# Kernel optimization log

Hardware: AMD Instinct MI355X
Metric: run time of the kernel (lower is better)

Reference implementation:

```python
import jax, jax.numpy as jnp
import numpy as np

N = 200000   # nodes
E = 500000   # edges
B = 4096     # batch of events
K = 20       # temporal neighbors
M = 100000   # pending raw messages
D = 128      # node feat / embedding dim
DT = 128     # time encoding dim (= D in TGN)
DM = 128     # memory dim
MSG = 128    # message dim
RAW = 2 * DM + D + DT   # 512 raw message dim
HID = RAW // 2          # 256 mlp hidden
HEADS = 2
QD = D + DT             # 256 attention query dim (= MHA embed_dim)
KD = D + DT + D         # 384 attention key dim (neigh feat + time + edge feat)
DH = QD // HEADS


def setup_inputs() -> dict:
    key = jax.random.key(0)
    ks = jax.random.split(key, 40)
    f = lambda i, shape, s=0.05: jax.random.normal(ks[i], shape, jnp.float32) * s
    ri = lambda i, shape, hi: jax.random.randint(ks[i], shape, 0, hi, jnp.int32)
    return {
        # event batch (int constants)
        'src_nodes': ri(0, (B,), N), 'dst_nodes': ri(1, (B,), N), 'neg_nodes': ri(2, (B,), N),
        'edge_times': ri(3, (B,), 1000000),
        # temporal neighbor lists for the 3B query nodes (neighbor_finder output)
        'neighbors': ri(4, (3 * B, K), N),
        'neighbor_edge_idxs': ri(5, (3 * B, K), E),
        'neighbor_edge_times': ri(6, (3 * B, K), 1000000),
        # pending raw message events ('last' aggregator picks last per node)
        'msg_src': ri(7, (M,), N), 'msg_dst': ri(8, (M,), N),
        'msg_eidx': ri(9, (M,), E), 'msg_t': ri(10, (M,), 1000000),
        'last_update': ri(11, (N,), 500000),
        # learned params / state (floats)
        'node_feats': f(12, (N, D)), 'edge_feats': f(13, (E, D)), 'memory': f(14, (N, DM)),
        'time_w': f(15, (DT,), 1.0), 'time_b': f(16, (DT,), 1.0),
        'msg_W1': f(17, (HID, RAW)), 'msg_b1': f(18, (HID,)),
        'msg_W2': f(19, (MSG, HID)), 'msg_b2': f(20, (MSG,)),
        'gru_Wi': f(21, (3 * DM, MSG)), 'gru_Wh': f(22, (3 * DM, DM)),
        'gru_bi': f(23, (3 * DM,)), 'gru_bh': f(24, (3 * DM,)),
        'Wq': f(25, (QD, QD)), 'bq': f(26, (QD,)),
        'Wk': f(27, (QD, KD)), 'bk': f(28, (QD,)),
        'Wv': f(29, (QD, KD)), 'bv': f(30, (QD,)),
        'Wo': f(31, (QD, QD)), 'bo': f(32, (QD,)),
        'mW1': f(33, (D, QD + D)), 'mb1': f(34, (D,)),
        'mW2': f(35, (D, D)), 'mb2': f(36, (D,)),
    }


def _time_enc(t, w, b):
    # TimeEncode: cos(t * w + b); t [...], out [..., DT]
    return jnp.cos(t[..., None] * w + b)


def _forward(node_feats, edge_feats, memory, time_w, time_b,
             msg_W1, msg_b1, msg_W2, msg_b2,
             gru_Wi, gru_Wh, gru_bi, gru_bh,
             Wq, bq, Wk, bk, Wv, bv, Wo, bo, mW1, mb1, mW2, mb2,
             src_nodes, dst_nodes, neg_nodes, edge_times,
             neighbors, neighbor_edge_idxs, neighbor_edge_times,
             msg_src, msg_dst, msg_eidx, msg_t, last_update):
    # ---- 1. get_updated_memory: 'last' aggregator + mlp message fn + GRU ----
    pos = jnp.arange(M, dtype=jnp.int32)
    last_pos = jnp.full((N,), -1, jnp.int32).at[msg_src].max(pos)  # last msg per node
    has_msg = last_pos >= 0
    idx = jnp.maximum(last_pos, 0)
    s, d = msg_src[idx], msg_dst[idx]
    e, t = msg_eidx[idx], msg_t[idx]
    dt = (t - last_update[s]).astype(jnp.float32)
    raw = jnp.concatenate([memory[s], memory[d], edge_feats[e],
                           _time_enc(dt, time_w, time_b)], axis=-1)  # [N, RAW]
    h1 = jax.nn.relu(raw @ msg_W1.T + msg_b1)
    msg = h1 @ msg_W2.T + msg_b2                                    # [N, MSG]
    # torch GRUCell (gate order r, z, n)
    gi = msg @ gru_Wi.T + gru_bi
    gh = memory @ gru_Wh.T + gru_bh
    ir, iz, inn = jnp.split(gi, 3, axis=-1)
    hr, hz, hn = jnp.split(gh, 3, axis=-1)
    r = jax.nn.sigmoid(ir + hr)
    z = jax.nn.sigmoid(iz + hz)
    n = jnp.tanh(inn + r * hn)
    new_mem = (1.0 - z) * n + z * memory
    mem_upd = jnp.where(has_msg[:, None], new_mem, memory)          # [N, DM]

    # ---- 2. graph-attention embedding (1 layer) over temporal neighbors ----
    nodes = jnp.concatenate([src_nodes, dst_nodes, neg_nodes])      # [3B]
    ts = jnp.tile(edge_times, 3).astype(jnp.float32)                # [3B]
    src_feat = mem_upd[nodes] + node_feats[nodes]                   # [3B, D]
    q_in = jnp.concatenate([src_feat,
                            _time_enc(jnp.zeros_like(ts), time_w, time_b)], -1)  # [3B, QD]
    pad_mask = neighbors == 0                                       # TGN: id 0 = padding
    n_feat = mem_upd[neighbors] + node_feats[neighbors]             # [3B, K, D]
    dt_n = ts[:, None] - neighbor_edge_times.astype(jnp.float32)
    k_in = jnp.concatenate([n_feat, _time_enc(dt_n, time_w, time_b),
                            edge_feats[neighbor_edge_idxs]], -1)    # [3B, K, KD]
    q = (q_in @ Wq.T + bq).reshape(-1, HEADS, DH)                   # [3B, H, DH]
    k = (k_in @ Wk.T + bk).reshape(-1, K, HEADS, DH)
    v = (k_in @ Wv.T + bv).reshape(-1, K, HEADS, DH)
    scores = jnp.einsum('bhd,bkhd->bhk', q, k) / jnp.sqrt(jnp.float32(DH))
    scores = jnp.where(pad_mask[:, None, :], -1e9, scores)
    attn = jax.nn.softmax(scores, axis=-1)                          # [3B, H, K]
    ctx = jnp.einsum('bhk,bkhd->bhd', attn, v).reshape(-1, QD)
    attn_out = ctx @ Wo.T + bo                                      # [3B, QD]
    all_masked = jnp.all(pad_mask, axis=-1)
    attn_out = jnp.where(all_masked[:, None], 0.0, attn_out)
    # MergeLayer(attn_out, src_feat)
    h = jax.nn.relu(jnp.concatenate([attn_out, src_feat], -1) @ mW1.T + mb1)
    emb = h @ mW2.T + mb2                                           # [3B, D]
    return emb.reshape(3, B, D)  # (source, destination, negative) embeddings


def reference(src_nodes, dst_nodes, neg_nodes, edge_times, neighbors,
              neighbor_edge_idxs, neighbor_edge_times, msg_src, msg_dst,
              msg_eidx, msg_t, last_update, node_feats, edge_feats, memory,
              time_w, time_b, msg_W1, msg_b1, msg_W2, msg_b2, gru_Wi, gru_Wh,
              gru_bi, gru_bh, Wq, bq, Wk, bk, Wv, bv, Wo, bo, mW1, mb1, mW2, mb2):
    return _forward(node_feats, edge_feats, memory, time_w, time_b,
                    msg_W1, msg_b1, msg_W2, msg_b2,
                    gru_Wi, gru_Wh, gru_bi, gru_bh,
                    Wq, bq, Wk, bk, Wv, bv, Wo, bo, mW1, mb1, mW2, mb2,
                    src_nodes, dst_nodes, neg_nodes, edge_times,
                    neighbors, neighbor_edge_idxs, neighbor_edge_times,
                    msg_src, msg_dst, msg_eidx, msg_t, last_update)
```

## Files before the change

kernel.cpp:

```cpp
#include <hip/hip_runtime.h>
#include <math.h>

#define NN 200000
#define EEDGE 500000
#define BB 4096
#define KK 20
#define MM 100000
#define Q3 (3*BB)
#define NBLK ((NN + 255) / 256)

typedef _Float16 __attribute__((ext_vector_type(8))) f16x8;
typedef _Float16 __attribute__((ext_vector_type(4))) f16x4;
typedef float __attribute__((ext_vector_type(4))) f32x4;

#define MFMA16(a,b,c) __builtin_amdgcn_mfma_f32_16x16x32_f16(a,b,c,0,0,0)

__device__ __forceinline__ float fast_cos(float a) {
    double ad = (double)a * 0.15915494309189535;
    double fr = ad - floor(ad);
    return __builtin_amdgcn_cosf((float)fr);
}

__device__ __forceinline__ float tenc(float dt, float w, float b) {
    float p = __fmul_rn(dt, w);
    float a = __fadd_rn(p, b);
    return fast_cos(a);
}

__device__ __forceinline__ float fsigm(float x) {
    return __builtin_amdgcn_rcpf(1.f + __expf(-x));
}
__device__ __forceinline__ float ftanh(float x) {
    return 1.f - 2.f * __builtin_amdgcn_rcpf(1.f + __expf(2.f * x));
}

__device__ __forceinline__ f32x4 z4() {
    f32x4 v; v[0] = 0.f; v[1] = 0.f; v[2] = 0.f; v[3] = 0.f; return v;
}

__global__ void k_init(int* lastpos, int* inv) {
    int i = blockIdx.x * 256 + threadIdx.x;
    if (i < NN) { lastpos[i] = -1; inv[i] = -1; }
}

__global__ void k_scatter(const int* __restrict__ msg_src, int* __restrict__ lastpos) {
    int i = blockIdx.x * 256 + threadIdx.x;
    if (i < MM) atomicMax(&lastpos[msg_src[i]], i);
}

__global__ void k_count(const int* __restrict__ lastpos, int* __restrict__ bcnt) {
    int n = blockIdx.x * 256 + threadIdx.x;
    int flag = (n < NN && lastpos[n] >= 0) ? 1 : 0;
    unsigned long long m = __ballot(flag != 0);
    __shared__ int wc[4];
    int wave = threadIdx.x >> 6, lane = threadIdx.x & 63;
    if (lane == 0) wc[wave] = __popcll(m);
    __syncthreads();
    if (threadIdx.x == 0) bcnt[blockIdx.x] = wc[0] + wc[1] + wc[2] + wc[3];
}

__global__ void k_scan(const int* __restrict__ bcnt, int* __restrict__ boff,
                       int* __restrict__ count) {
    __shared__ int s[NBLK];
    int t = threadIdx.x;
    for (int i = t; i < NBLK; i += 256) s[i] = bcnt[i];
    __syncthreads();
    if (t == 0) {
        int acc = 0;
        for (int i = 0; i < NBLK; i++) { int v = s[i]; s[i] = acc; acc += v; }
        *count = acc;
    }
    __syncthreads();
    for (int i = t; i < NBLK; i += 256) boff[i] = s[i];
}

__global__ void k_fill(const int* __restrict__ lastpos, const int* __restrict__ boff,
                       int* __restrict__ comp, int* __restrict__ inv) {
    int n = blockIdx.x * 256 + threadIdx.x;
    int flag = (n < NN && lastpos[n] >= 0) ? 1 : 0;
    unsigned long long m = __ballot(flag != 0);
    __shared__ int wc[4];
    int wave = threadIdx.x >> 6, lane = threadIdx.x & 63;
    if (lane == 0) wc[wave] = __popcll(m);
    __syncthreads();
    int base = boff[blockIdx.x];
    for (int i = 0; i < wave; i++) base += wc[i];
    int rank = __popcll(m & ((1ull << lane) - 1));
    if (flag) {
        int pos = base + rank;
        comp[pos] = n;
        inv[n] = pos;
    }
}

__global__ void k_cvtw(const float* __restrict__ W1, const float* __restrict__ W2,
                       const float* __restrict__ Wi, const float* __restrict__ Wh,
                       const float* __restrict__ Wq, const float* __restrict__ Wv,
                       const float* __restrict__ Wo, const float* __restrict__ mW1,
                       const float* __restrict__ mW2, const float* __restrict__ Wk,
                       _Float16* __restrict__ dst) {
    int f = blockIdx.x * 256 + threadIdx.x;
    if (f >= 81920) return;
    const float* src; int dstoff, K, lf, tr = -1;
    if      (f < 16384) { src = W1;  dstoff = 0;      K = 512; lf = f; }
    else if (f < 20480) { src = W2;  dstoff = 131072; K = 256; lf = f - 16384; }
    else if (f < 26624) { src = Wi;  dstoff = 163840; K = 128; lf = f - 20480; }
    else if (f < 32768) { src = Wh;  dstoff = 212992; K = 128; lf = f - 26624; }
    else if (f < 40960) { src = Wq;  dstoff = 262144; K = 256; lf = f - 32768; }
    else if (f < 47104) { src = Wv;  dstoff = 327680; K = 384; lf = f - 40960; }
    else if (f < 53248) { src = Wv + 128 * 384; dstoff = 376832; K = 384; lf = f - 47104; }
    else if (f < 61440) { src = Wo;  dstoff = 425984; K = 256; lf = f - 53248; }
    else if (f < 67584) { src = mW1; dstoff = 491520; K = 384; lf = f - 61440; }
    else if (f < 69632) { src = mW2; dstoff = 540672; K = 128; lf = f - 67584; }
    else if (f < 75776) { src = Wk;  dstoff = 557056; K = 128; lf = f - 69632; tr = 0; }
    else                { src = Wk;  dstoff = 606208; K = 128; lf = f - 75776; tr = 1; }
    int KS = K >> 5;
    int cgrp = lf / (KS * 64);
    int rem  = lf - cgrp * (KS * 64);
    int ks = rem >> 6, lane = rem & 63;
    int kg = lane >> 4, arow = lane & 15;
    int col = cgrp * 16 + arow;
    int k0 = ks * 32 + kg * 8;
    f16x8 h;
    if (tr < 0) {
        const float* p = src + (size_t)col * K + k0;
        float4 a = *(const float4*)p;
        float4 b = *(const float4*)(p + 4);
        h[0] = (_Float16)a.x; h[1] = (_Float16)a.y; h[2] = (_Float16)a.z; h[3] = (_Float16)a.w;
        h[4] = (_Float16)b.x; h[5] = (_Float16)b.y; h[6] = (_Float16)b.z; h[7] = (_Float16)b.w;
    } else {
        #pragma unroll
        for (int e = 0; e < 8; e++)
            h[e] = (_Float16)Wk[(size_t)(tr * 128 + k0 + e) * 384 + col];
    }
    *(f16x8*)(dst + dstoff + (size_t)lf * 8) = h;
}

__device__ __forceinline__ int SWA(int r, int byteofs) {
    return r * 1024 + (byteofs ^ ((r & 7) << 4));
}

__device__ __forceinline__ f16x8 ldw4(const _Float16* W, int cg, int ks, int lane) {
    return *(const f16x8*)(W + (((size_t)cg * 4 + ks) * 64 + lane) * 8);
}

__global__ __launch_bounds__(512, 2)
void k_stage1(const int* __restrict__ comp, const int* __restrict__ count,
              const int* __restrict__ lastpos,
              const int* __restrict__ msg_dst, const int* __restrict__ msg_eidx,
              const int* __restrict__ msg_t, const int* __restrict__ last_update,
              const float* __restrict__ memory, const float* __restrict__ edge_feats,
              const float* __restrict__ time_w, const float* __restrict__ time_b,
              const _Float16* __restrict__ W1h, const float* __restrict__ b1,
              const _Float16* __restrict__ W2h, const float* __restrict__ b2,
              const _Float16* __restrict__ Wih, const _Float16* __restrict__ Whh,
              const float* __restrict__ bi, const float* __restrict__ bh,
              _Float16* __restrict__ new_mem)
{
    __shared__ char rawb[64 * 1024];
    __shared__ int sn[64], sd[64], se[64];
    __shared__ float sdt[64];

    int cnt = *count;
    int r0 = blockIdx.x * 64;
    if (r0 >= cnt) return;
    int tid = threadIdx.x;

    if (tid < 64) {
        int rr = r0 + tid;
        int j = (rr < cnt) ? rr : r0;
        int n = comp[j];
        int idx = lastpos[n];
        sn[tid] = n;
        sd[tid] = msg_dst[idx];
        se[tid] = msg_eidx[idx];
        sdt[tid] = (float)(msg_t[idx] - last_update[n]);
    }
    __syncthreads();

    #pragma unroll
    for (int it = 0; it < 6; it++) {
        int gi = tid + it * 512;
        int r = gi / 48, g = gi - r * 48;
        const float* src;
        if (g < 16)      src = memory + (size_t)sn[r] * 128 + g * 8;
        else if (g < 32) src = memory + (size_t)sd[r] * 128 + (g - 16) * 8;
        else             src = edge_feats + (size_t)se[r] * 128 + (g - 32) * 8;
        float4 a = *(const float4*)src;
        float4 b = *(const float4*)(src + 4);
        f16x8 h;
        h[0] = (_Float16)a.x; h[1] = (_Float16)a.y; h[2] = (_Float16)a.z; h[3] = (_Float16)a.w;
        h[4] = (_Float16)b.x; h[5] = (_Float16)b.y; h[6] = (_Float16)b.z; h[7] = (_Float16)b.w;
        *(f16x8*)(rawb + SWA(r, g * 16)) = h;
    }
    #pragma unroll
    for (int it = 0; it < 2; it++) {
        int gi = tid + it * 512;
        int r = gi >> 4, g = gi & 15;
        int c = g * 8;
        float dt = sdt[r];
        float4 w0 = *(const float4*)(time_w + c);
        float4 w1 = *(const float4*)(time_w + c + 4);
        float4 t0 = *(const float4*)(time_b + c);
        float4 t1 = *(const float4*)(time_b + c + 4);
        f16x8 h;
        h[0] = (_Float16)tenc(dt, w0.x, t0.x); h[1] = (_Float16)tenc(dt, w0.y, t0.y);
        h[2] = (_Float16)tenc(dt, w0.z, t0.z); h[3] = (_Float16)tenc(dt, w0.w, t0.w);
        h[4] = (_Float16)tenc(dt, w1.x, t1.x); h[5] = (_Float16)tenc(dt, w1.y, t1.y);
        h[6] = (_Float16)tenc(dt, w1.z, t1.z); h[7] = (_Float16)tenc(dt, w1.w, t1.w);
        *(f16x8*)(rawb + SWA(r, (48 + g) * 16)) = h;
    }
    __syncthreads();

    int wv = tid >> 6, lane = tid & 63;
    int arow = lane & 15, kg = lane >> 4;

    f32x4 acc1[2][4];
    #pragma unroll
    for (int c = 0; c < 2; c++)
        #pragma unroll
        for (int rt = 0; rt < 4; rt++) acc1[c][rt] = z4();
    for (int ks = 0; ks < 16; ks++) {
        f16x8 a[4];
        #pragma unroll
        for (int rt = 0; rt < 4; rt++)
            a[rt] = *(const f16x8*)(rawb + SWA(rt * 16 + arow, ks * 64 + kg * 16));
        #pragma unroll
        for (int c = 0; c < 2; c++) {
            f16x8 b = *(const f16x8*)(W1h + (((size_t)(wv * 2 + c) * 16 + ks) * 64 + lane) * 8);
            #pragma unroll
            for (int rt = 0; rt < 4; rt++)
                acc1[c][rt] = MFMA16(a[rt], b, acc1[c][rt]);
        }
    }
    __syncthreads();

    #pragma unroll
    for (int c = 0; c < 2; c++) {
        int col = (wv * 2 + c) * 16 + arow;
        float bb = b1[col];
        #pragma unroll
        for (int rt = 0; rt < 4; rt++)
            #pragma unroll
            for (int rg = 0; rg < 4; rg++) {
                int row = rt * 16 + kg * 4 + rg;
                float v = fmaxf(acc1[c][rt][rg] + bb, 0.f);
                *(_Float16*)(rawb + SWA(row, 384 + col * 2)) = (_Float16)v;
            }
    }
    __syncthreads();

    f32x4 acc2[4];
    #pragma unroll
    for (int rt = 0; rt < 4; rt++) acc2[rt] = z4();
    for (int ks = 0; ks < 8; ks++) {
        f16x8 b = *(const f16x8*)(W2h + (((size_t)wv * 8 + ks) * 64 + lane) * 8);
        #pragma unroll
        for (int rt = 0; rt < 4; rt++) {
            f16x8 a = *(const f16x8*)(rawb + SWA(rt * 16 + arow, 384 + ks * 64 + kg * 16));
            acc2[rt] = MFMA16(a, b, acc2[rt]);
        }
    }
    __syncthreads();

    {
        int col = wv * 16 + arow;
        float bb = b2[col];
        #pragma unroll
        for (int rt = 0; rt < 4; rt++)
            #pragma unroll
            for (int rg = 0; rg < 4; rg++) {
                int row = rt * 16 + kg * 4 + rg;
                *(_Float16*)(rawb + SWA(row, 384 + col * 2)) =
                    (_Float16)(acc2[rt][rg] + bb);
            }
    }
    __syncthreads();

    f32x4 aR[4], aZ[4], aNi[4], aNh[4];
    #pragma unroll
    for (int rt = 0; rt < 4; rt++) { aR[rt] = z4(); aZ[rt] = z4(); aNi[rt] = z4(); aNh[rt] = z4(); }
    for (int ks = 0; ks < 4; ks++) {
        f16x8 bi_ = ldw4(Wih, wv, ks, lane);
        f16x8 bh_ = ldw4(Whh, wv, ks, lane);
        #pragma unroll
        for (int rt = 0; rt < 4; rt++) {
            f16x8 m = *(const f16x8*)(rawb + SWA(rt * 16 + arow, 384 + ks * 64 + kg * 16));
            f16x8 hh = *(const f16x8*)(rawb + SWA(rt * 16 + arow, ks * 64 + kg * 16));
            aR[rt] = MFMA16(m, bi_, aR[rt]);
            aR[rt] = MFMA16(hh, bh_, aR[rt]);
        }
    }
    for (int ks = 0; ks < 4; ks++) {
        f16x8 bi_ = ldw4(Wih, 8 + wv, ks, lane);
        f16x8 bh_ = ldw4(Whh, 8 + wv, ks, lane);
        #pragma unroll
        for (int rt = 0; rt < 4; rt++) {
            f16x8 m = *(const f16x8*)(rawb + SWA(rt * 16 + arow, 384 + ks * 64 + kg * 16));
            f16x8 hh = *(const f16x8*)(rawb + SWA(rt * 16 + arow, ks * 64 + kg * 16));
            aZ[rt] = MFMA16(m, bi_, aZ[rt]);
            aZ[rt] = MFMA16(hh, bh_, aZ[rt]);
        }
    }
    for (int ks = 0; ks < 4; ks++) {
        f16x8 bi_ = ldw4(Wih, 16 + wv, ks, lane);
        f16x8 bh_ = ldw4(Whh, 16 + wv, ks, lane);
        #pragma unroll
        for (int rt = 0; rt < 4; rt++) {
            f16x8 m = *(const f16x8*)(rawb + SWA(rt * 16 + arow, 384 + ks * 64 + kg * 16));
            f16x8 hh = *(const f16x8*)(rawb + SWA(rt * 16 + arow, ks * 64 + kg * 16));
            aNi[rt] = MFMA16(m, bi_, aNi[rt]);
            aNh[rt] = MFMA16(hh, bh_, aNh[rt]);
        }
    }

    {
        int col = wv * 16 + arow;
        float bir = bi[col],        bhr = bh[col];
        float biz = bi[128 + col],  bhz = bh[128 + col];
        float bin_ = bi[256 + col], bhn_ = bh[256 + col];
        #pragma unroll
        for (int rt = 0; rt < 4; rt++)
            #pragma unroll
            for (int rg = 0; rg < 4; rg++) {
                int row = rt * 16 + kg * 4 + rg;
                int rr = r0 + row;
                if (rr < cnt) {
                    float r_ = fsigm(aR[rt][rg] + bir + bhr);
                    float zg = fsigm(aZ[rt][rg] + biz + bhz);
                    float ng = ftanh(aNi[rt][rg] + bin_ + r_ * (aNh[rt][rg] + bhn_));
                    float om = (float)*(const _Float16*)(rawb + SWA(row, col * 2));
                    new_mem[(size_t)rr * 128 + col] = (_Float16)((1.f - zg) * ng + zg * om);
                }
            }
    }
}

__global__ __launch_bounds__(256)
void k_feat(const int* __restrict__ inv, const _Float16* __restrict__ new_mem,
            const float* __restrict__ memory, const float* __restrict__ node_feats,
            _Float16* __restrict__ feat)
{
    int idx = blockIdx.x * 256 + threadIdx.x;
    if (idx >= NN * 16) return;
    int n = idx >> 4, g = idx & 15;
    int c = g * 8;
    int iv = inv[n];
    float4 n0 = *(const float4*)(node_feats + (size_t)n * 128 + c);
    float4 n1 = *(const float4*)(node_feats + (size_t)n * 128 + c + 4);
    f16x8 o;
    if (iv >= 0) {
        f16x8 mv = *(const f16x8*)(new_mem + (size_t)iv * 128 + c);
        o[0] = (_Float16)((float)mv[0] + n0.x); o[1] = (_Float16)((float)mv[1] + n0.y);
        o[2] = (_Float16)((float)mv[2] + n0.z); o[3] = (_Float16)((float)mv[3] + n0.w);
        o[4] = (_Float16)((float)mv[4] + n1.x); o[5] = (_Float16)((float)mv[5] + n1.y);
        o[6] = (_Float16)((float)mv[6] + n1.z); o[7] = (_Float16)((float)mv[7] + n1.w);
    } else {
        float4 m0 = *(const float4*)(memory + (size_t)n * 128 + c);
        float4 m1 = *(const float4*)(memory + (size_t)n * 128 + c + 4);
        o[0] = (_Float16)(m0.x + n0.x); o[1] = (_Float16)(m0.y + n0.y);
        o[2] = (_Float16)(m0.z + n0.z); o[3] = (_Float16)(m0.w + n0.w);
        o[4] = (_Float16)(m1.x + n1.x); o[5] = (_Float16)(m1.y + n1.y);
        o[6] = (_Float16)(m1.z + n1.z); o[7] = (_Float16)(m1.w + n1.w);
    }
    *(f16x8*)(feat + (size_t)n * 128 + c) = o;
}

__global__ void k2a(const int* __restrict__ src_nodes, const int* __restrict__ dst_nodes,
                    const int* __restrict__ neg_nodes, const _Float16* __restrict__ feat,
                    const float* __restrict__ time_b,
                    _Float16* __restrict__ q_in, _Float16* __restrict__ acat)
{
    __shared__ int snode[32];
    int tid = threadIdx.x;
    int r0 = blockIdx.x * 32;
    if (tid < 32) {
        int q = r0 + tid;
        snode[tid] = (q < BB) ? src_nodes[q] : (q < 2 * BB) ? dst_nodes[q - BB] : neg_nodes[q - 2 * BB];
    }
    __syncthreads();
    #pragma unroll
    for (int it = 0; it < 4; it++) {
        int gi = tid + it * 256;
        int r = gi >> 5, ch = gi & 31;
        int c = ch * 4;
        int node = snode[r];
        f16x4 sf = *(const f16x4*)(feat + (size_t)node * 128 + c);
        size_t q = (size_t)(r0 + r);
        *(f16x4*)(q_in + q * 256 + c) = sf;
        *(f16x4*)(acat + q * 384 + 256 + c) = sf;
        float4 tb = *(const float4*)(time_b + c);
        f16x4 te;
        te[0] = (_Float16)fast_cos(tb.x); te[1] = (_Float16)fast_cos(tb.y);
        te[2] = (_Float16)fast_cos(tb.z); te[3] = (_Float16)fast_cos(tb.w);
        *(f16x4*)(q_in + q * 256 + 128 + c) = te;
    }
}

__global__ __launch_bounds__(512, 2)
void k2b(const _Float16* __restrict__ q_in, const _Float16* __restrict__ Wqh,
         const float* __restrict__ bq, const _Float16* __restrict__ Wkth,
         _Float16* __restrict__ qk_ws)
{
    __shared__ char lds[32 * 1024];
    int tid = threadIdx.x;
    int r0 = blockIdx.x * 32;

    #pragma unroll
    for (int t = 0; t < 2; t++) {
        int gi = tid + t * 512;
        int r = gi >> 5, g = gi & 31;
        f16x8 v = *(const f16x8*)(q_in + (size_t)(r0 + r) * 256 + g * 8);
        *(f16x8*)(&lds[r * 512 + ((g * 16) ^ ((r & 7) << 4))]) = v;
    }
    __syncthreads();

    int wv = tid >> 6, lane = tid & 63;
    int arow = lane & 15, kg = lane >> 4;

    f32x4 acc[2][2];
    #pragma unroll
    for (int c = 0; c < 2; c++) { acc[c][0] = z4(); acc[c][1] = z4(); }
    for (int ks = 0; ks < 8; ks++) {
        f16x8 a0 = *(const f16x8*)(&lds[arow * 512 + ((ks * 64 + kg * 16) ^ ((arow & 7) << 4))]);
        f16x8 a1 = *(const f16x8*)(&lds[(16 + arow) * 512 + ((ks * 64 + kg * 16) ^ ((arow & 7) << 4))]);
        #pragma unroll
        for (int c = 0; c < 2; c++) {
            f16x8 b = *(const f16x8*)(Wqh + (((size_t)(wv * 2 + c) * 8 + ks) * 64 + lane) * 8);
            acc[c][0] = MFMA16(a0, b, acc[c][0]);
            acc[c][1] = MFMA16(a1, b, acc[c][1]);
        }
    }
    #pragma unroll
    for (int c = 0; c < 2; c++) {
        int col = (wv * 2 + c) * 16 + arow;
        float bb = bq[col];
        #pragma unroll
        for (int rt = 0; rt < 2; rt++)
            #pragma unroll
            for (int rg = 0; rg < 4; rg++) {
                int row = rt * 16 + kg * 4 + rg;
                *(_Float16*)(&lds[16384 + row * 512 + ((col * 2) ^ ((row & 7) << 4))]) =
                    (_Float16)(acc[c][rt][rg] + bb);
            }
    }
    __syncthreads();

    int h = wv >> 2;
    f32x4 acc2[6][2];
    #pragma unroll
    for (int c = 0; c < 6; c++) { acc2[c][0] = z4(); acc2[c][1] = z4(); }
    for (int ks = 0; ks < 4; ks++) {
        f16x8 a0 = *(const f16x8*)(&lds[16384 + arow * 512 +
                    ((h * 256 + ks * 64 + kg * 16) ^ ((arow & 7) << 4))]);
        f16x8 a1 = *(const f16x8*)(&lds[16384 + (16 + arow) * 512 +
                    ((h * 256 + ks * 64 + kg * 16) ^ ((arow & 7) << 4))]);
        #pragma unroll
        for (int c = 0; c < 6; c++) {
            int cgh = (wv & 3) * 6 + c;
            f16x8 b = *(const f16x8*)(Wkth + (size_t)h * 49152 +
                       (((size_t)cgh * 4 + ks) * 64 + lane) * 8);
            acc2[c][0] = MFMA16(a0, b, acc2[c][0]);
            acc2[c][1] = MFMA16(a1, b, acc2[c][1]);
        }
    }
    #pragma unroll
    for (int c = 0; c < 6; c++) {
        int cgh = (wv & 3) * 6 + c;
        int col = h * 384 + cgh * 16 + arow;
        #pragma unroll
        for (int rt = 0; rt < 2; rt++)
            #pragma unroll
            for (int rg = 0; rg < 4; rg++) {
                int row = rt * 16 + kg * 4 + rg;
                qk_ws[(size_t)(r0 + row) * 768 + col] = (_Float16)acc2[c][rt][rg];
            }
    }
}

template<int KD, int NFRAG, bool RELU>
__global__ __launch_bounds__(256, 4)
void k_gemm(const _Float16* __restrict__ A, int lda, int a_ys,
            const _Float16* __restrict__ B, int b_ys,
            const float* __restrict__ bias, int bias_ys,
            _Float16* __restrict__ C, int ldc, int c_ys,
            float* __restrict__ C32,
            const int* __restrict__ rowmask)
{
    constexpr int ROWB = KD * 2;
    __shared__ char As[32 * ROWB];
    int tid = threadIdx.x;
    int r0 = blockIdx.x * 32;
    int aoff = blockIdx.y * a_ys;
    const _Float16* Bp = B + (size_t)blockIdx.y * b_ys;
    int coff = blockIdx.y * c_ys;

    #pragma unroll
    for (int t = 0; t < (32 * KD / 8) / 256; t++) {
        int gi = tid + t * 256;
        int r = gi / (KD / 8), g = gi % (KD / 8);
        f16x8 v = *(const f16x8*)(A + (size_t)(r0 + r) * lda + aoff + g * 8);
        *(f16x8*)(&As[r * ROWB + ((g * 16) ^ ((r & 7) << 4))]) = v;
    }
    __syncthreads();

    int wv = tid >> 6, lane = tid & 63;
    int arow = lane & 15, kg = lane >> 4;
    f32x4 acc[NFRAG][2];
    #pragma unroll
    for (int c = 0; c < NFRAG; c++) { acc[c][0] = z4(); acc[c][1] = z4(); }

    #pragma unroll
    for (int ks = 0; ks < KD / 32; ks++) {
        f16x8 a0 = *(const f16x8*)(&As[arow * ROWB + ((ks * 64 + kg * 16) ^ ((arow & 7) << 4))]);
        f16x8 a1 = *(const f16x8*)(&As[(16 + arow) * ROWB + ((ks * 64 + kg * 16) ^ ((arow & 7) << 4))]);
        #pragma unroll
        for (int c = 0; c < NFRAG; c++) {
            f16x8 b = *(const f16x8*)(Bp +
                (((size_t)(wv * NFRAG + c) * (KD / 32) + ks) * 64 + lane) * 8);
            acc[c][0] = MFMA16(a0, b, acc[c][0]);
            acc[c][1] = MFMA16(a1, b, acc[c][1]);
        }
    }

    #pragma unroll
    for (int c = 0; c < NFRAG; c++) {
        int cg = (wv * NFRAG + c) * 16 + arow;
        float bb = bias ? bias[blockIdx.y * bias_ys + cg] : 0.f;
        #pragma unroll
        for (int rt = 0; rt < 2; rt++)
            #pragma unroll
            for (int rg = 0; rg < 4; rg++) {
                int grow = r0 + rt * 16 + kg * 4 + rg;
                float v = acc[c][rt][rg] + bb;
                if (RELU) v = fmaxf(v, 0.f);
                if (rowmask && rowmask[grow]) v = 0.f;
                if (C)   C[(size_t)grow * ldc + coff + cg] = (_Float16)v;
                if (C32) C32[(size_t)grow * ldc + coff + cg] = v;
            }
    }
}

__global__ __launch_bounds__(256)
void k2d(const int* __restrict__ neighbors, const int* __restrict__ nb_eidx,
         const int* __restrict__ nb_et, const int* __restrict__ edge_times,
         const _Float16* __restrict__ feat,
         const float* __restrict__ edge_feats, const float* __restrict__ time_w,
         const float* __restrict__ time_b,
         _Float16* __restrict__ qk_wsum, int* __restrict__ allm)
{
    int tid = threadIdx.x;
    int qi = blockIdx.x * 4 + (tid >> 6);
    int lane = tid & 63;
    int h = lane >> 5, l32 = lane & 31;
    int c0 = l32 * 4;

    float4 tw = *(const float4*)(time_w + c0);
    float4 tb = *(const float4*)(time_b + c0);

    const _Float16* qkp = qk_wsum + (size_t)qi * 768 + h * 384;
    f16x4 t0 = *(const f16x4*)(qkp + c0);
    f16x4 t1 = *(const f16x4*)(qkp + 128 + c0);
    f16x4 t2 = *(const f16x4*)(qkp + 256 + c0);
    float qk0[4], qk1[4], qk2[4];
    #pragma unroll
    for (int t = 0; t < 4; t++) { qk0[t] = (float)t0[t]; qk1[t] = (float)t1[t]; qk2[t] = (float)t2[t]; }

    float ts = (float)edge_times[qi & (BB - 1)];
    float m_run = -3.0e38f, l_run = 0.f;
    float w0[4] = {0,0,0,0}, w1[4] = {0,0,0,0}, w2[4] = {0,0,0,0};
    int anyv = 0;
    const float inv_sqrt = 0.08838834764831845f;

    int base = qi * KK;
    int nb_c = neighbors[base];
    int ei_c = nb_eidx[base];
    int et_c = nb_et[base];
    f16x4 fv;
    float4 ef;
    {
        fv = *(const f16x4*)(feat + (size_t)nb_c * 128 + c0);
        ef = *(const float4*)(edge_feats + (size_t)ei_c * 128 + c0);
    }

    for (int j = 0; j < KK; j++) {
        int nb_n = 0, ei_n = 0, et_n = 0;
        f16x4 fv_n = {0,0,0,0};
        float4 ef_n = {0,0,0,0};
        if (j + 1 < KK) {
            nb_n = neighbors[base + j + 1];
            ei_n = nb_eidx[base + j + 1];
            et_n = nb_et[base + j + 1];
            fv_n = *(const f16x4*)(feat + (size_t)nb_n * 128 + c0);
            ef_n = *(const float4*)(edge_feats + (size_t)ei_n * 128 + c0);
        }

        float dtf = ts - (float)et_c;
        anyv |= (nb_c != 0);
        float k0[4] = { (float)fv[0], (float)fv[1], (float)fv[2], (float)fv[3] };
        float k1[4] = { tenc(dtf, tw.x, tb.x), tenc(dtf, tw.y, tb.y),
                        tenc(dtf, tw.z, tb.z), tenc(dtf, tw.w, tb.w) };
        float k2[4] = { ef.x, ef.y, ef.z, ef.w };

        float sp = 0.f;
        #pragma unroll
        for (int t = 0; t < 4; t++)
            sp += qk0[t] * k0[t] + qk1[t] * k1[t] + qk2[t] * k2[t];
        sp += __shfl_xor(sp, 1, 32);
        sp += __shfl_xor(sp, 2, 32);
        sp += __shfl_xor(sp, 4, 32);
        sp += __shfl_xor(sp, 8, 32);
        sp += __shfl_xor(sp, 16, 32);

        float s = sp * inv_sqrt;
        if (nb_c == 0) s = -1e9f;
        float m_new = fmaxf(m_run, s);
        float sc = __expf(m_run - m_new);
        float p = __expf(s - m_new);
        l_run = l_run * sc + p;
        #pragma unroll
        for (int t = 0; t < 4; t++) {
            w0[t] = w0[t] * sc + p * k0[t];
            w1[t] = w1[t] * sc + p * k1[t];
            w2[t] = w2[t] * sc + p * k2[t];
        }
        m_run = m_new;

        nb_c = nb_n; ei_c = ei_n; et_c = et_n;
        fv = fv_n; ef = ef_n;
    }

    float linv = __builtin_amdgcn_rcpf(l_run);
    _Float16* wp = qk_wsum + (size_t)qi * 768 + h * 384;
    f16x4 o0, o1, o2;
    #pragma unroll
    for (int t = 0; t < 4; t++) {
        o0[t] = (_Float16)(w0[t] * linv);
        o1[t] = (_Float16)(w1[t] * linv);
        o2[t] = (_Float16)(w2[t] * linv);
    }
    *(f16x4*)(wp + c0) = o0;
    *(f16x4*)(wp + 128 + c0) = o1;
    *(f16x4*)(wp + 256 + c0) = o2;
    if (lane == 0) allm[qi] = anyv ? 0 : 1;
}

extern "C" void kernel_launch(void* const* d_in, const int* in_sizes, int n_in,
                              void* d_out, int out_size, void* d_ws, size_t ws_size,
                              hipStream_t stream) {
    (void)in_sizes; (void)n_in; (void)out_size; (void)ws_size;
    const int* src_nodes  = (const int*)d_in[0];
    const int* dst_nodes  = (const int*)d_in[1];
    const int* neg_nodes  = (const int*)d_in[2];
    const int* edge_times = (const int*)d_in[3];
    const int* neighbors  = (const int*)d_in[4];
    const int* nb_eidx    = (const int*)d_in[5];
    const int* nb_et      = (const int*)d_in[6];
    const int* msg_src    = (const int*)d_in[7];
    const int* msg_dst    = (const int*)d_in[8];
    const int* msg_eidx   = (const int*)d_in[9];
    const int* msg_t      = (const int*)d_in[10];
    const int* last_update= (const int*)d_in[11];
    const float* node_feats = (const float*)d_in[12];
    const float* edge_feats = (const float*)d_in[13];
    const float* memory     = (const float*)d_in[14];
    const float* time_w = (const float*)d_in[15];
    const float* time_b = (const float*)d_in[16];
    const float* W1 = (const float*)d_in[17];
    const float* b1 = (const float*)d_in[18];
    const float* W2 = (const float*)d_in[19];
    const float* b2 = (const float*)d_in[20];
    const float* gWi = (const float*)d_in[21];
    const float* gWh = (const float*)d_in[22];
    const float* gbi = (const float*)d_in[23];
    const float* gbh = (const float*)d_in[24];
    const float* Wq = (const float*)d_in[25];
    const float* bq = (const float*)d_in[26];
    const float* Wk = (const float*)d_in[27];
    const float* bk = (const float*)d_in[28];
    const float* Wv = (const float*)d_in[29];
    const float* bv = (const float*)d_in[30];
    const float* Wo = (const float*)d_in[31];
    const float* bo = (const float*)d_in[32];
    const float* mW1 = (const float*)d_in[33];
    const float* mb1 = (const float*)d_in[34];
    const float* mW2 = (const float*)d_in[35];
    const float* mb2 = (const float*)d_in[36];
    float* out = (float*)d_out;
    (void)bk;

    char* w = (char*)d_ws;
    int* lastpos = (int*)w;
    int* inv  = lastpos + NN;
    int* comp = inv + NN;
    int* count = comp + NN;
    int* bcnt = count + 1;
    int* boff = bcnt + NBLK;
    size_t off = ((size_t)(3 * NN + 1 + 2 * NBLK) * 4 + 255) & ~(size_t)255;
    _Float16* new_mem = (_Float16*)(w + off);
    size_t foff = off + (size_t)MM * 128 * 2;
    _Float16* feat = (_Float16*)(w + foff);
    size_t woff = foff + (size_t)NN * 128 * 2;

    _Float16* Hpool = (_Float16*)(w + woff);
    _Float16* W1h  = Hpool;
    _Float16* W2h  = Hpool + 131072;
    _Float16* Wih  = Hpool + 163840;
    _Float16* Whh  = Hpool + 212992;
    _Float16* Wqh  = Hpool + 262144;
    _Float16* Wvh  = Hpool + 327680;
    _Float16* Woh  = Hpool + 425984;
    _Float16* mW1h = Hpool + 491520;
    _Float16* mW2h = Hpool + 540672;
    _Float16* Wkth = Hpool + 557056;
    size_t boff2 = woff + (size_t)655360 * 2;

    _Float16* qin_ctx = (_Float16*)(w + boff2);
    _Float16* q_hm    = qin_ctx + (size_t)Q3 * 256;
    _Float16* qk_ws   = q_hm + (size_t)Q3 * 256;
    _Float16* acat    = qk_ws + (size_t)Q3 * 768;
    int* allm         = (int*)(acat + (size_t)Q3 * 384);

    k_init<<<dim3(NBLK), dim3(256), 0, stream>>>(lastpos, inv);
    k_scatter<<<dim3((MM + 255) / 256), dim3(256), 0, stream>>>(msg_src, lastpos);
    k_count<<<dim3(NBLK), dim3(256), 0, stream>>>(lastpos, bcnt);
    k_scan<<<dim3(1), dim3(256), 0, stream>>>(bcnt, boff, count);
    k_fill<<<dim3(NBLK), dim3(256), 0, stream>>>(lastpos, boff, comp, inv);
    k_cvtw<<<dim3(320), dim3(256), 0, stream>>>(W1, W2, gWi, gWh, Wq, Wv, Wo, mW1, mW2, Wk, Hpool);
    k_stage1<<<dim3((MM + 63) / 64), dim3(512), 0, stream>>>(
        comp, count, lastpos, msg_dst, msg_eidx, msg_t, last_update,
        memory, edge_feats, time_w, time_b,
        W1h, b1, W2h, b2, Wih, Whh, gbi, gbh, new_mem);
    k_feat<<<dim3(NN * 16 / 256), dim3(256), 0, stream>>>(
        inv, new_mem, memory, node_feats, feat);

    k2a<<<dim3(Q3 / 32), dim3(256), 0, stream>>>(
        src_nodes, dst_nodes, neg_nodes, feat, time_b, qin_ctx, acat);
    k2b<<<dim3(Q3 / 32), dim3(512), 0, stream>>>(
        qin_ctx, Wqh, bq, Wkth, qk_ws);
    k2d<<<dim3(Q3 / 4), dim3(256), 0, stream>>>(
        neighbors, nb_eidx, nb_et, edge_times, feat,
        edge_feats, time_w, time_b, qk_ws, allm);
    k_gemm<384, 2, false><<<dim3(Q3 / 32, 2), dim3(256), 0, stream>>>(
        qk_ws, 768, 384, Wvh, 128 * 384, bv, 128, qin_ctx, 256, 128, nullptr, nullptr);
    k_gemm<256, 4, false><<<dim3(Q3 / 32, 1), dim3(256), 0, stream>>>(
        qin_ctx, 256, 0, Woh, 0, bo, 0, acat, 384, 0, nullptr, allm);
    k_gemm<384, 2, true><<<dim3(Q3 / 32, 1), dim3(256), 0, stream>>>(
        acat, 384, 0, mW1h, 0, mb1, 0, q_hm, 128, 0, nullptr, nullptr);
    k_gemm<128, 2, false><<<dim3(Q3 / 32, 1), dim3(256), 0, stream>>>(
        q_hm, 128, 0, mW2h, 0, mb2, 0, nullptr, 128, 0, out, nullptr);
}
```

Measured before the change: 308.1 us.

## Compute node features only for referenced nodes, fold time bias into Wq, fuse tail GEMMs

```diff
diff --git a/kernel.cpp b/kernel.cpp
--- a/kernel.cpp
+++ b/kernel.cpp
@@ -38,14 +38,27 @@
     f32x4 v; v[0] = 0.f; v[1] = 0.f; v[2] = 0.f; v[3] = 0.f; return v;
 }
 
-__global__ void k_init(int* lastpos, int* inv) {
+__global__ void k_init(int* lastpos, int* inv, char* mask) {
     int i = blockIdx.x * 256 + threadIdx.x;
-    if (i < NN) { lastpos[i] = -1; inv[i] = -1; }
+    if (i < NN) { lastpos[i] = -1; inv[i] = -1; mask[i] = 0; }
 }
 
 __global__ void k_scatter(const int* __restrict__ msg_src, int* __restrict__ lastpos) {
     int i = blockIdx.x * 256 + threadIdx.x;
     if (i < MM) atomicMax(&lastpos[msg_src[i]], i);
+}
+
+__global__ void k_mark(const int* __restrict__ src_nodes, const int* __restrict__ dst_nodes,
+                       const int* __restrict__ neg_nodes, const int* __restrict__ neighbors,
+                       char* __restrict__ mask) {
+    int i = blockIdx.x * 256 + threadIdx.x;
+    if (i < Q3) {
+        int node = (i < BB) ? src_nodes[i] : (i < 2 * BB) ? dst_nodes[i - BB] : neg_nodes[i - 2 * BB];
+        mask[node] = 1;
+    } else {
+        int e = i - Q3;
+        if (e < Q3 * KK) mask[neighbors[e]] = 1;
+    }
 }
 
 __global__ void k_count(const int* __restrict__ lastpos, int* __restrict__ bcnt) {
@@ -93,6 +106,19 @@
     }
 }
 
+__global__ void k_prep(const float* __restrict__ Wq, const float* __restrict__ bq,
+                       const float* __restrict__ time_b, float* __restrict__ bq2) {
+    __shared__ float cte[128];
+    int t = threadIdx.x;
+    if (t < 128) cte[t] = fast_cos(time_b[t]);
+    __syncthreads();
+    float acc = bq[t];
+    #pragma unroll 4
+    for (int d = 0; d < 128; d++)
+        acc += Wq[(size_t)t * 256 + 128 + d] * cte[d];
+    bq2[t] = acc;
+}
+
 __global__ void k_cvtw(const float* __restrict__ W1, const float* __restrict__ W2,
                        const float* __restrict__ Wi, const float* __restrict__ Wh,
                        const float* __restrict__ Wq, const float* __restrict__ Wv,
@@ -100,20 +126,20 @@
                        const float* __restrict__ mW2, const float* __restrict__ Wk,
                        _Float16* __restrict__ dst) {
     int f = blockIdx.x * 256 + threadIdx.x;
-    if (f >= 81920) return;
-    const float* src; int dstoff, K, lf, tr = -1;
-    if      (f < 16384) { src = W1;  dstoff = 0;      K = 512; lf = f; }
-    else if (f < 20480) { src = W2;  dstoff = 131072; K = 256; lf = f - 16384; }
-    else if (f < 26624) { src = Wi;  dstoff = 163840; K = 128; lf = f - 20480; }
-    else if (f < 32768) { src = Wh;  dstoff = 212992; K = 128; lf = f - 26624; }
-    else if (f < 40960) { src = Wq;  dstoff = 262144; K = 256; lf = f - 32768; }
-    else if (f < 47104) { src = Wv;  dstoff = 327680; K = 384; lf = f - 40960; }
-    else if (f < 53248) { src = Wv + 128 * 384; dstoff = 376832; K = 384; lf = f - 47104; }
-    else if (f < 61440) { src = Wo;  dstoff = 425984; K = 256; lf = f - 53248; }
-    else if (f < 67584) { src = mW1; dstoff = 491520; K = 384; lf = f - 61440; }
-    else if (f < 69632) { src = mW2; dstoff = 540672; K = 128; lf = f - 67584; }
-    else if (f < 75776) { src = Wk;  dstoff = 557056; K = 128; lf = f - 69632; tr = 0; }
-    else                { src = Wk;  dstoff = 606208; K = 128; lf = f - 75776; tr = 1; }
+    if (f >= 77824) return;
+    const float* src; int dstoff, K, ldb, lf, tr = -1;
+    if      (f < 16384) { src = W1;  dstoff = 0;      K = 512; ldb = 512; lf = f; }
+    else if (f < 20480) { src = W2;  dstoff = 131072; K = 256; ldb = 256; lf = f - 16384; }
+    else if (f < 26624) { src = Wi;  dstoff = 163840; K = 128; ldb = 128; lf = f - 20480; }
+    else if (f < 32768) { src = Wh;  dstoff = 212992; K = 128; ldb = 128; lf = f - 26624; }
+    else if (f < 36864) { src = Wq;  dstoff = 262144; K = 128; ldb = 256; lf = f - 32768; }
+    else if (f < 43008) { src = Wv;  dstoff = 294912; K = 384; ldb = 384; lf = f - 36864; }
+    else if (f < 49152) { src = Wv + 128 * 384; dstoff = 344064; K = 384; ldb = 384; lf = f - 43008; }
+    else if (f < 57344) { src = Wo;  dstoff = 393216; K = 256; ldb = 256; lf = f - 49152; }
+    else if (f < 63488) { src = mW1; dstoff = 458752; K = 384; ldb = 384; lf = f - 57344; }
+    else if (f < 65536) { src = mW2; dstoff = 507904; K = 128; ldb = 128; lf = f - 63488; }
+    else if (f < 71680) { src = Wk;  dstoff = 524288; K = 128; ldb = 0; lf = f - 65536; tr = 0; }
+    else                { src = Wk;  dstoff = 573440; K = 128; ldb = 0; lf = f - 71680; tr = 1; }
     int KS = K >> 5;
     int cgrp = lf / (KS * 64);
     int rem  = lf - cgrp * (KS * 64);
@@ -123,7 +149,7 @@
     int k0 = ks * 32 + kg * 8;
     f16x8 h;
     if (tr < 0) {
-        const float* p = src + (size_t)col * K + k0;
+        const float* p = src + (size_t)col * ldb + k0;
         float4 a = *(const float4*)p;
         float4 b = *(const float4*)(p + 4);
         h[0] = (_Float16)a.x; h[1] = (_Float16)a.y; h[2] = (_Float16)a.z; h[3] = (_Float16)a.w;
@@ -337,13 +363,15 @@
 }
 
 __global__ __launch_bounds__(256)
-void k_feat(const int* __restrict__ inv, const _Float16* __restrict__ new_mem,
+void k_feat(const int* __restrict__ inv, const char* __restrict__ mask,
+            const _Float16* __restrict__ new_mem,
             const float* __restrict__ memory, const float* __restrict__ node_feats,
             _Float16* __restrict__ feat)
 {
     int idx = blockIdx.x * 256 + threadIdx.x;
     if (idx >= NN * 16) return;
     int n = idx >> 4, g = idx & 15;
+    if (!mask[n]) return;
     int c = g * 8;
     int iv = inv[n];
     float4 n0 = *(const float4*)(node_feats + (size_t)n * 128 + c);
@@ -366,52 +394,29 @@
     *(f16x8*)(feat + (size_t)n * 128 + c) = o;
 }
 
-__global__ void k2a(const int* __restrict__ src_nodes, const int* __restrict__ dst_nodes,
-                    const int* __restrict__ neg_nodes, const _Float16* __restrict__ feat,
-                    const float* __restrict__ time_b,
-                    _Float16* __restrict__ q_in, _Float16* __restrict__ acat)
+__global__ __launch_bounds__(512, 2)
+void k2b(const int* __restrict__ src_nodes, const int* __restrict__ dst_nodes,
+         const int* __restrict__ neg_nodes, const _Float16* __restrict__ feat,
+         const _Float16* __restrict__ WqLh, const float* __restrict__ bq2,
+         const _Float16* __restrict__ Wkth,
+         _Float16* __restrict__ sfeat, _Float16* __restrict__ qk_ws)
 {
+    __shared__ char lds[24 * 1024];
     __shared__ int snode[32];
     int tid = threadIdx.x;
     int r0 = blockIdx.x * 32;
+
     if (tid < 32) {
         int q = r0 + tid;
         snode[tid] = (q < BB) ? src_nodes[q] : (q < 2 * BB) ? dst_nodes[q - BB] : neg_nodes[q - 2 * BB];
     }
     __syncthreads();
-    #pragma unroll
-    for (int it = 0; it < 4; it++) {
-        int gi = tid + it * 256;
-        int r = gi >> 5, ch = gi & 31;
-        int c = ch * 4;
-        int node = snode[r];
-        f16x4 sf = *(const f16x4*)(feat + (size_t)node * 128 + c);
-        size_t q = (size_t)(r0 + r);
-        *(f16x4*)(q_in + q * 256 + c) = sf;
-        *(f16x4*)(acat + q * 384 + 256 + c) = sf;
-        float4 tb = *(const float4*)(time_b + c);
-        f16x4 te;
-        te[0] = (_Float16)fast_cos(tb.x); te[1] = (_Float16)fast_cos(tb.y);
-        te[2] = (_Float16)fast_cos(tb.z); te[3] = (_Float16)fast_cos(tb.w);
-        *(f16x4*)(q_in + q * 256 + 128 + c) = te;
-    }
-}
-
-__global__ __launch_bounds__(512, 2)
-void k2b(const _Float16* __restrict__ q_in, const _Float16* __restrict__ Wqh,
-         const float* __restrict__ bq, const _Float16* __restrict__ Wkth,
-         _Float16* __restrict__ qk_ws)
-{
-    __shared__ char lds[32 * 1024];
-    int tid = threadIdx.x;
-    int r0 = blockIdx.x * 32;
-
-    #pragma unroll
-    for (int t = 0; t < 2; t++) {
-        int gi = tid + t * 512;
-        int r = gi >> 5, g = gi & 31;
-        f16x8 v = *(const f16x8*)(q_in + (size_t)(r0 + r) * 256 + g * 8);
-        *(f16x8*)(&lds[r * 512 + ((g * 16) ^ ((r & 7) << 4))]) = v;
+
+    {
+        int r = tid >> 4, g = tid & 15;
+        f16x8 v = *(const f16x8*)(feat + (size_t)snode[r] * 128 + g * 8);
+        *(f16x8*)(&lds[r * 256 + ((g * 16) ^ ((r & 7) << 4))]) = v;
+        *(f16x8*)(sfeat + (size_t)(r0 + r) * 128 + g * 8) = v;
     }
     __syncthreads();
 
@@ -421,12 +426,12 @@
     f32x4 acc[2][2];
     #pragma unroll
     for (int c = 0; c < 2; c++) { acc[c][0] = z4(); acc[c][1] = z4(); }
-    for (int ks = 0; ks < 8; ks++) {
-        f16x8 a0 = *(const f16x8*)(&lds[arow * 512 + ((ks * 64 + kg * 16) ^ ((arow & 7) << 4))]);
-        f16x8 a1 = *(const f16x8*)(&lds[(16 + arow) * 512 + ((ks * 64 + kg * 16) ^ ((arow & 7) << 4))]);
+    for (int ks = 0; ks < 4; ks++) {
+        f16x8 a0 = *(const f16x8*)(&lds[arow * 256 + ((ks * 64 + kg * 16) ^ ((arow & 7) << 4))]);
+        f16x8 a1 = *(const f16x8*)(&lds[(16 + arow) * 256 + ((ks * 64 + kg * 16) ^ ((arow & 7) << 4))]);
         #pragma unroll
         for (int c = 0; c < 2; c++) {
-            f16x8 b = *(const f16x8*)(Wqh + (((size_t)(wv * 2 + c) * 8 + ks) * 64 + lane) * 8);
+            f16x8 b = *(const f16x8*)(WqLh + (((size_t)(wv * 2 + c) * 4 + ks) * 64 + lane) * 8);
             acc[c][0] = MFMA16(a0, b, acc[c][0]);
             acc[c][1] = MFMA16(a1, b, acc[c][1]);
         }
@@ -434,13 +439,13 @@
     #pragma unroll
     for (int c = 0; c < 2; c++) {
         int col = (wv * 2 + c) * 16 + arow;
-        float bb = bq[col];
+        float bb = bq2[col];
         #pragma unroll
         for (int rt = 0; rt < 2; rt++)
             #pragma unroll
             for (int rg = 0; rg < 4; rg++) {
                 int row = rt * 16 + kg * 4 + rg;
-                *(_Float16*)(&lds[16384 + row * 512 + ((col * 2) ^ ((row & 7) << 4))]) =
+                *(_Float16*)(&lds[8192 + row * 512 + ((col * 2) ^ ((row & 7) << 4))]) =
                     (_Float16)(acc[c][rt][rg] + bb);
             }
     }
@@ -451,9 +456,9 @@
     #pragma unroll
     for (int c = 0; c < 6; c++) { acc2[c][0] = z4(); acc2[c][1] = z4(); }
     for (int ks = 0; ks < 4; ks++) {
-        f16x8 a0 = *(const f16x8*)(&lds[16384 + arow * 512 +
+        f16x8 a0 = *(const f16x8*)(&lds[8192 + arow * 512 +
                     ((h * 256 + ks * 64 + kg * 16) ^ ((arow & 7) << 4))]);
-        f16x8 a1 = *(const f16x8*)(&lds[16384 + (16 + arow) * 512 +
+        f16x8 a1 = *(const f16x8*)(&lds[8192 + (16 + arow) * 512 +
                     ((h * 256 + ks * 64 + kg * 16) ^ ((arow & 7) << 4))]);
         #pragma unroll
         for (int c = 0; c < 6; c++) {
@@ -643,6 +648,119 @@
     *(f16x4*)(wp + 128 + c0) = o1;
     *(f16x4*)(wp + 256 + c0) = o2;
     if (lane == 0) allm[qi] = anyv ? 0 : 1;
+}
+
+__global__ __launch_bounds__(256, 2)
+void k2t2(const _Float16* __restrict__ ctx, const _Float16* __restrict__ sfeat,
+          const _Float16* __restrict__ Woh, const float* __restrict__ bo,
+          const _Float16* __restrict__ mW1h, const float* __restrict__ mb1,
+          const _Float16* __restrict__ mW2h, const float* __restrict__ mb2,
+          const int* __restrict__ allm, float* __restrict__ out)
+{
+    __shared__ char lds[48 * 1024];
+    int tid = threadIdx.x;
+    int r0 = blockIdx.x * 32;
+
+    #pragma unroll
+    for (int t = 0; t < 4; t++) {
+        int gi = tid + t * 256;
+        int r = gi >> 5, g = gi & 31;
+        f16x8 v = *(const f16x8*)(ctx + (size_t)(r0 + r) * 256 + g * 8);
+        *(f16x8*)(&lds[r * 512 + ((g * 16) ^ ((r & 7) << 4))]) = v;
+    }
+    __syncthreads();
+
+    int wv = tid >> 6, lane = tid & 63;
+    int arow = lane & 15, kg = lane >> 4;
+
+    f32x4 acc[4][2];
+    #pragma unroll
+    for (int c = 0; c < 4; c++) { acc[c][0] = z4(); acc[c][1] = z4(); }
+    for (int ks = 0; ks < 8; ks++) {
+        f16x8 a0 = *(const f16x8*)(&lds[arow * 512 + ((ks * 64 + kg * 16) ^ ((arow & 7) << 4))]);
+        f16x8 a1 = *(const f16x8*)(&lds[(16 + arow) * 512 + ((ks * 64 + kg * 16) ^ ((arow & 7) << 4))]);
+        #pragma unroll
+        for (int c = 0; c < 4; c++) {
+            f16x8 b = *(const f16x8*)(Woh + (((size_t)(wv * 4 + c) * 8 + ks) * 64 + lane) * 8);
+            acc[c][0] = MFMA16(a0, b, acc[c][0]);
+            acc[c][1] = MFMA16(a1, b, acc[c][1]);
+        }
+    }
+    #pragma unroll
+    for (int c = 0; c < 4; c++) {
+        int col = (wv * 4 + c) * 16 + arow;
+        float bb = bo[col];
+        #pragma unroll
+        for (int rt = 0; rt < 2; rt++)
+            #pragma unroll
+            for (int rg = 0; rg < 4; rg++) {
+                int row = rt * 16 + kg * 4 + rg;
+                float v = allm[r0 + row] ? 0.f : (acc[c][rt][rg] + bb);
+                *(_Float16*)(&lds[16384 + row * 768 + ((col * 2) ^ ((row & 7) << 4))]) = (_Float16)v;
+            }
+    }
+    #pragma unroll
+    for (int t = 0; t < 2; t++) {
+        int gi = tid + t * 256;
+        int r = gi >> 4, g = gi & 15;
+        f16x8 v = *(const f16x8*)(sfeat + (size_t)(r0 + r) * 128 + g * 8);
+        *(f16x8*)(&lds[16384 + r * 768 + ((512 + g * 16) ^ ((r & 7) << 4))]) = v;
+    }
+    __syncthreads();
+
+    f32x4 acc2[2][2];
+    #pragma unroll
+    for (int c = 0; c < 2; c++) { acc2[c][0] = z4(); acc2[c][1] = z4(); }
+    for (int ks = 0; ks < 12; ks++) {
+        f16x8 a0 = *(const f16x8*)(&lds[16384 + arow * 768 + ((ks * 64 + kg * 16) ^ ((arow & 7) << 4))]);
+        f16x8 a1 = *(const f16x8*)(&lds[16384 + (16 + arow) * 768 + ((ks * 64 + kg * 16) ^ ((arow & 7) << 4))]);
+        #pragma unroll
+        for (int c = 0; c < 2; c++) {
+            f16x8 b = *(const f16x8*)(mW1h + (((size_t)(wv * 2 + c) * 12 + ks) * 64 + lane) * 8);
+            acc2[c][0] = MFMA16(a0, b, acc2[c][0]);
+            acc2[c][1] = MFMA16(a1, b, acc2[c][1]);
+        }
+    }
+    #pragma unroll
+    for (int c = 0; c < 2; c++) {
+        int col = (wv * 2 + c) * 16 + arow;
+        float bb = mb1[col];
+        #pragma unroll
+        for (int rt = 0; rt < 2; rt++)
+            #pragma unroll
+            for (int rg = 0; rg < 4; rg++) {
+                int row = rt * 16 + kg * 4 + rg;
+                float v = fmaxf(acc2[c][rt][rg] + bb, 0.f);
+                *(_Float16*)(&lds[40960 + row * 256 + ((col * 2) ^ ((row & 7) << 4))]) = (_Float16)v;
+            }
+    }
+    __syncthreads();
+
+    f32x4 acc3[2][2];
+    #pragma unroll
+    for (int c = 0; c < 2; c++) { acc3[c][0] = z4(); acc3[c][1] = z4(); }
+    for (int ks = 0; ks < 4; ks++) {
+        f16x8 a0 = *(const f16x8*)(&lds[40960 + arow * 256 + ((ks * 64 + kg * 16) ^ ((arow & 7) << 4))]);
+        f16x8 a1 = *(const f16x8*)(&lds[40960 + (16 + arow) * 256 + ((ks * 64 + kg * 16) ^ ((arow & 7) << 4))]);
+        #pragma unroll
+        for (int c = 0; c < 2; c++) {
+            f16x8 b = *(const f16x8*)(mW2h + (((size_t)(wv * 2 + c) * 4 + ks) * 64 + lane) * 8);
+            acc3[c][0] = MFMA16(a0, b, acc3[c][0]);
+            acc3[c][1] = MFMA16(a1, b, acc3[c][1]);
+        }
+    }
+    #pragma unroll
+    for (int c = 0; c < 2; c++) {
+        int col = (wv * 2 + c) * 16 + arow;
+        float bb = mb2[col];
+        #pragma unroll
+        for (int rt = 0; rt < 2; rt++)
+            #pragma unroll
+            for (int rg = 0; rg < 4; rg++) {
+                int row = rt * 16 + kg * 4 + rg;
+                out[(size_t)(r0 + row) * 128 + col] = acc3[c][rt][rg] + bb;
+            }
+    }
 }
 
 extern "C" void kernel_launch(void* const* d_in, const int* in_sizes, int n_in,
@@ -696,7 +814,8 @@
     int* count = comp + NN;
     int* bcnt = count + 1;
     int* boff = bcnt + NBLK;
-    size_t off = ((size_t)(3 * NN + 1 + 2 * NBLK) * 4 + 255) & ~(size_t)255;
+    char* mask = (char*)(boff + NBLK);
+    size_t off = ((size_t)(3 * NN + 1 + 2 * NBLK) * 4 + NN + 255) & ~(size_t)255;
     _Float16* new_mem = (_Float16*)(w + off);
     size_t foff = off + (size_t)MM * 128 * 2;
     _Float16* feat = (_Float16*)(w + foff);
@@ -707,46 +826,43 @@
     _Float16* W2h  = Hpool + 131072;
     _Float16* Wih  = Hpool + 163840;
     _Float16* Whh  = Hpool + 212992;
-    _Float16* Wqh  = Hpool + 262144;
-    _Float16* Wvh  = Hpool + 327680;
-    _Float16* Woh  = Hpool + 425984;
-    _Float16* mW1h = Hpool + 491520;
-    _Float16* mW2h = Hpool + 540672;
-    _Float16* Wkth = Hpool + 557056;
-    size_t boff2 = woff + (size_t)655360 * 2;
-
-    _Float16* qin_ctx = (_Float16*)(w + boff2);
-    _Float16* q_hm    = qin_ctx + (size_t)Q3 * 256;
-    _Float16* qk_ws   = q_hm + (size_t)Q3 * 256;
-    _Float16* acat    = qk_ws + (size_t)Q3 * 768;
-    int* allm         = (int*)(acat + (size_t)Q3 * 384);
-
-    k_init<<<dim3(NBLK), dim3(256), 0, stream>>>(lastpos, inv);
+    _Float16* WqLh = Hpool + 262144;
+    _Float16* Wvh  = Hpool + 294912;
+    _Float16* Woh  = Hpool + 393216;
+    _Float16* mW1h = Hpool + 458752;
+    _Float16* mW2h = Hpool + 507904;
+    _Float16* Wkth = Hpool + 524288;
+    float* bq2 = (float*)(Hpool + 622592);
+    size_t boff2 = woff + (size_t)622592 * 2 + 1024;
+
+    _Float16* ctx   = (_Float16*)(w + boff2);
+    _Float16* qk_ws = ctx + (size_t)Q3 * 256;
+    _Float16* sfeat = qk_ws + (size_t)Q3 * 768;
+    int* allm       = (int*)(sfeat + (size_t)Q3 * 128);
+
+    k_init<<<dim3(NBLK), dim3(256), 0, stream>>>(lastpos, inv, mask);
     k_scatter<<<dim3((MM + 255) / 256), dim3(256), 0, stream>>>(msg_src, lastpos);
+    k_mark<<<dim3((Q3 + Q3 * KK + 255) / 256), dim3(256), 0, stream>>>(
+        src_nodes, dst_nodes, neg_nodes, neighbors, mask);
     k_count<<<dim3(NBLK), dim3(256), 0, stream>>>(lastpos, bcnt);
     k_scan<<<dim3(1), dim3(256), 0, stream>>>(bcnt, boff, count);
     k_fill<<<dim3(NBLK), dim3(256), 0, stream>>>(lastpos, boff, comp, inv);
-    k_cvtw<<<dim3(320), dim3(256), 0, stream>>>(W1, W2, gWi, gWh, Wq, Wv, Wo, mW1, mW2, Wk, Hpool);
+    k_cvtw<<<dim3(304), dim3(256), 0, stream>>>(W1, W2, gWi, gWh, Wq, Wv, Wo, mW1, mW2, Wk, Hpool);
+    k_prep<<<dim3(1), dim3(256), 0, stream>>>(Wq, bq, time_b, bq2);
     k_stage1<<<dim3((MM + 63) / 64), dim3(512), 0, stream>>>(
         comp, count, lastpos, msg_dst, msg_eidx, msg_t, last_update,
         memory, edge_feats, time_w, time_b,
         W1h, b1, W2h, b2, Wih, Whh, gbi, gbh, new_mem);
     k_feat<<<dim3(NN * 16 / 256), dim3(256), 0, stream>>>(
-        inv, new_mem, memory, node_feats, feat);
-
-    k2a<<<dim3(Q3 / 32), dim3(256), 0, stream>>>(
-        src_nodes, dst_nodes, neg_nodes, feat, time_b, qin_ctx, acat);
+        inv, mask, new_mem, memory, node_feats, feat);
+
     k2b<<<dim3(Q3 / 32), dim3(512), 0, stream>>>(
-        qin_ctx, Wqh, bq, Wkth, qk_ws);
+        src_nodes, dst_nodes, neg_nodes, feat, WqLh, bq2, Wkth, sfeat, qk_ws);
     k2d<<<dim3(Q3 / 4), dim3(256), 0, stream>>>(
         neighbors, nb_eidx, nb_et, edge_times, feat,
         edge_feats, time_w, time_b, qk_ws, allm);
     k_gemm<384, 2, false><<<dim3(Q3 / 32, 2), dim3(256), 0, stream>>>(
-        qk_ws, 768, 384, Wvh, 128 * 384, bv, 128, qin_ctx, 256, 128, nullptr, nullptr);
-    k_gemm<256, 4, false><<<dim3(Q3 / 32, 1), dim3(256), 0, stream>>>(
-        qin_ctx, 256, 0, Woh, 0, bo, 0, acat, 384, 0, nullptr, allm);
-    k_gemm<384, 2, true><<<dim3(Q3 / 32, 1), dim3(256), 0, stream>>>(
-        acat, 384, 0, mW1h, 0, mb1, 0, q_hm, 128, 0, nullptr, nullptr);
-    k_gemm<128, 2, false><<<dim3(Q3 / 32, 1), dim3(256), 0, stream>>>(
-        q_hm, 128, 0, mW2h, 0, mb2, 0, nullptr, 128, 0, out, nullptr);
-}
+        qk_ws, 768, 384, Wvh, 49152, bv, 128, ctx, 256, 128, nullptr, nullptr);
+    k2t2<<<dim3(Q3 / 32), dim3(256), 0, stream>>>(
+        ctx, sfeat, Woh, bo, mW1h, mb1, mW2h, mb2, allm, out);
+}
```

New measurement: 284.4 us. 7.7% less time.
